# Kernel tuning notes

Measured on AMD Instinct MI355X. Metric: run time of the kernel, lower is better.

## Reference

```python
import jax, jax.numpy as jnp
import numpy as np

N_NODES = 100000
N_EDGES = 800000
IN_DIM = 128
HIDDEN = 128
CLASSES = 40


def _glorot(key, shape):
    fan_in, fan_out = shape
    lim = (6.0 / (fan_in + fan_out)) ** 0.5
    return jax.random.uniform(key, shape, jnp.float32, -lim, lim)


def setup_inputs() -> dict:
    key = jax.random.key(0)
    ks = jax.random.split(key, 8)
    x = jax.random.normal(ks[0], (N_NODES, IN_DIM), jnp.float32)
    edge_index = jax.random.randint(ks[1], (2, N_EDGES), 0, N_NODES, jnp.int64)
    # SAGEConv layer 1: lin_l (neighbor, with bias), lin_r (root, no bias)
    W1_l = _glorot(ks[2], (IN_DIM, HIDDEN))
    W1_r = _glorot(ks[3], (IN_DIM, HIDDEN))
    b1 = jnp.zeros((HIDDEN,), jnp.float32)
    # SAGEConv layer 2
    W2_l = _glorot(ks[4], (HIDDEN, CLASSES))
    W2_r = _glorot(ks[5], (HIDDEN, CLASSES))
    b2 = jnp.zeros((CLASSES,), jnp.float32)
    return {"x": x, "edge_index": edge_index, "W1_l": W1_l, "W1_r": W1_r,
            "b1": b1, "W2_l": W2_l, "W2_r": W2_r, "b2": b2}


def _sage_conv(x, src, dst, W_l, W_r, b):
    # mean aggregation of source-node features into destination nodes
    msgs = x[src]                                             # [E, d] gather
    agg = jax.ops.segment_sum(msgs, dst, num_segments=N_NODES)  # [N, d]
    cnt = jax.ops.segment_sum(jnp.ones((src.shape[0],), x.dtype), dst,
                              num_segments=N_NODES)           # [N]
    mean = agg / jnp.maximum(cnt, 1.0)[:, None]
    return mean @ W_l + x @ W_r + b


def reference(x, edge_index, W1_l, W1_r, b1, W2_l, W2_r, b2):
    src, dst = edge_index[0], edge_index[1]
    h = _sage_conv(x, src, dst, W1_l, W1_r, b1)
    h = jax.nn.relu(h)
    # F.dropout in eval mode is the identity (deterministic reference)
    out = _sage_conv(h, src, dst, W2_l, W2_r, b2)
    return out
```

## Files before the change

kernel.cpp:

```cpp
#include <hip/hip_runtime.h>
#include <hip/hip_bf16.h>

#define N_NODES 100000
#define N_EDGES 800000
#define IN_DIM  128
#define HIDDEN  128
#define CLASSES 40
#define CAP     32
#define NSH     8
#define SLICES  100
#define EPB     8000
#define BIN_B   (NSH*SLICES)
#define CAST_B  12500
#define PACK_B  24
#define CUR_STRIDE 12544

typedef __attribute__((ext_vector_type(8))) short bf16x8;
typedef __attribute__((ext_vector_type(4))) float floatx4;
typedef __attribute__((ext_vector_type(4))) int intx4;
typedef __attribute__((ext_vector_type(4))) unsigned short ushortx4;

__device__ __forceinline__ float bf2f(unsigned short u) {
    return __uint_as_float(((unsigned int)u) << 16);
}
__device__ __forceinline__ unsigned short f2bf(float f) {
    unsigned int u = __float_as_uint(f);
    unsigned int r = 0x7fffu + ((u >> 16) & 1u);
    return (unsigned short)((u + r) >> 16);
}
__device__ __forceinline__ int curIdx(int d) { return (d & 7) * CUR_STRIDE + (d >> 3); }

__global__ void k_prep(const int* __restrict__ src, const int* __restrict__ dst,
                       int* __restrict__ cur, int* __restrict__ csr,
                       const float* __restrict__ x, unsigned short* __restrict__ A1,
                       const float* __restrict__ W1l, const float* __restrict__ W1r,
                       unsigned short* __restrict__ Bp1,
                       const float* __restrict__ W2l, const float* __restrict__ W2r,
                       unsigned short* __restrict__ Bp2) {
    int blk = blockIdx.x;
    if (blk < BIN_B) {
        int g = blk & 7;
        int slice = blk >> 3;
        const intx4* s4p = reinterpret_cast<const intx4*>(src) + slice * (EPB / 4);
        const intx4* d4p = reinterpret_cast<const intx4*>(dst) + slice * (EPB / 4);
        for (int i = threadIdx.x; i < EPB / 4; i += 256) {
            intx4 d4 = __builtin_nontemporal_load(d4p + i);
            intx4 s4 = __builtin_nontemporal_load(s4p + i);
            #pragma unroll
            for (int j = 0; j < 4; ++j) {
                int d = d4[j];
                if ((d & 7) == g) {
                    int s = s4[j];
                    int slot = atomicAdd(&cur[g * CUR_STRIDE + (d >> 3)], 1);
                    if (slot < CAP) csr[d * CAP + slot] = s;
                }
            }
        }
    } else if (blk < BIN_B + CAST_B) {
        int t = (blk - BIN_B) * 256 + threadIdx.x;
        int n = t >> 5, g = t & 31;
        floatx4 v = __builtin_nontemporal_load(
            reinterpret_cast<const floatx4*>(x + (size_t)n * 128) + g);
        ushortx4 u = { f2bf(v.x), f2bf(v.y), f2bf(v.z), f2bf(v.w) };
        __builtin_nontemporal_store(u,
            reinterpret_cast<ushortx4*>(A1 + (size_t)n * 256 + 128 + g * 4));
    } else {
        int t = (blk - BIN_B - CAST_B) * 256 + threadIdx.x;
        if (t < 4096) {
            int o = t >> 7, n = t & 127;
            const float* W = (o < 16) ? W1l : W1r;
            int k0 = (o & 15) * 8;
            union { unsigned short us[8]; uint4 v; } pk;
            #pragma unroll
            for (int j = 0; j < 8; ++j) pk.us[j] = f2bf(W[(size_t)(k0 + j) * 128 + n]);
            *(uint4*)(Bp1 + (size_t)t * 8) = pk.v;
        } else {
            int t2 = t - 4096;
            int o = t2 >> 7, n = t2 & 127;
            const float* W = (n < 64) ? W2l : W2r;
            int col = n & 63;
            int k0 = o * 8;
            union { unsigned short us[8]; uint4 v; } pk;
            #pragma unroll
            for (int j = 0; j < 8; ++j)
                pk.us[j] = (col < 40) ? f2bf(W[(size_t)(k0 + j) * 40 + col]) : (unsigned short)0;
            *(uint4*)(Bp2 + (size_t)t2 * 8) = pk.v;
        }
    }
}

__global__ void k_agg1(unsigned short* __restrict__ A1, const int* __restrict__ deg,
                       const int* __restrict__ csr) {
    int n = blockIdx.x * 4 + (threadIdx.x >> 6);
    int lane = threadIdx.x & 63;
    if (n >= N_NODES) return;
    int cnt = min(deg[curIdx(n)], CAP);
    int nl = csr[n * CAP + (lane & (CAP - 1))];
    int r = lane >> 4, c = lane & 15;
    float acc[8] = {0.f, 0.f, 0.f, 0.f, 0.f, 0.f, 0.f, 0.f};
    for (int base = 0; base < cnt; base += 16) {
        #pragma unroll
        for (int u = 0; u < 4; ++u) {
            int e = base + u * 4 + r;
            int s = __shfl(nl, min(e, cnt - 1) & 31, 64);
            bf16x8 v = {};
            if (e < cnt)
                v = *(const bf16x8*)(A1 + (size_t)s * 256 + 128 + c * 8);
            #pragma unroll
            for (int j = 0; j < 8; ++j) acc[j] += bf2f((unsigned short)v[j]);
        }
    }
    #pragma unroll
    for (int j = 0; j < 8; ++j) {
        acc[j] += __shfl_xor(acc[j], 16, 64);
        acc[j] += __shfl_xor(acc[j], 32, 64);
    }
    if (lane < 16) {
        float inv = 1.0f / fmaxf((float)cnt, 1.0f);
        union { unsigned short us[8]; bf16x8 v; } pk;
        #pragma unroll
        for (int j = 0; j < 8; ++j) pk.us[j] = f2bf(acc[j] * inv);
        *(bf16x8*)(A1 + (size_t)n * 256 + c * 8) = pk.v;
    }
}

__global__ __launch_bounds__(256)
void k_gemm(unsigned short* __restrict__ A1, const unsigned short* __restrict__ Bp1,
            const float* __restrict__ b1, const unsigned short* __restrict__ Bp2) {
    __shared__ unsigned short Hs[4][16][136];
    int wv = threadIdx.x >> 6, lane = threadIdx.x & 63;
    int q = lane >> 4, nn = lane & 15;
    int m0 = blockIdx.x * 64 + wv * 16;
    int ma = m0 + nn;
    bool mv = (ma < N_NODES);
    const unsigned short* arow = A1 + (size_t)ma * 256;

    floatx4 acc[8] = {};
    for (int kt = 0; kt < 8; ++kt) {
        bf16x8 a = {};
        if (mv) a = *(const bf16x8*)(arow + kt * 32 + q * 8);
        bf16x8 b[8];
        #pragma unroll
        for (int nt = 0; nt < 8; ++nt)
            b[nt] = *(const bf16x8*)(Bp1 + ((size_t)((kt * 4 + q) * 128 + nt * 16 + nn)) * 8);
        #pragma unroll
        for (int nt = 0; nt < 8; ++nt)
            acc[nt] = __builtin_amdgcn_mfma_f32_16x16x32_bf16(a, b[nt], acc[nt], 0, 0, 0);
    }
    #pragma unroll
    for (int nt = 0; nt < 8; ++nt) {
        int col = nt * 16 + nn;
        float bias = b1[col];
        #pragma unroll
        for (int r = 0; r < 4; ++r)
            Hs[wv][q * 4 + r][col] = f2bf(fmaxf(acc[nt][r] + bias, 0.f));
    }
    floatx4 acc2[8] = {};
    for (int kt = 0; kt < 4; ++kt) {
        bf16x8 a = *(const bf16x8*)(&Hs[wv][nn][kt * 32 + q * 8]);
        bf16x8 b[8];
        #pragma unroll
        for (int nt = 0; nt < 8; ++nt)
            b[nt] = *(const bf16x8*)(Bp2 + ((size_t)((kt * 4 + q) * 128 + nt * 16 + nn)) * 8);
        #pragma unroll
        for (int nt = 0; nt < 8; ++nt)
            acc2[nt] = __builtin_amdgcn_mfma_f32_16x16x32_bf16(a, b[nt], acc2[nt], 0, 0, 0);
    }
    #pragma unroll
    for (int nt = 0; nt < 4; ++nt) {
        int col = nt * 16 + nn;
        #pragma unroll
        for (int r = 0; r < 4; ++r) {
            int ro = m0 + q * 4 + r;
            if (ro < N_NODES)
                A1[(size_t)ro * 256 + col] = f2bf(acc2[nt][r]);
        }
    }
    #pragma unroll
    for (int nt = 4; nt < 8; ++nt) {
        int col = (nt - 4) * 16 + nn;
        #pragma unroll
        for (int r = 0; r < 4; ++r) {
            int ro = m0 + q * 4 + r;
            if (ro < N_NODES) {
                float* Rp = (float*)(A1 + (size_t)ro * 256 + 128);
                Rp[col] = acc2[nt][r];
            }
        }
    }
}

__global__ void k_agg2(const unsigned short* __restrict__ A1, const int* __restrict__ deg,
                       const int* __restrict__ csr, const float* __restrict__ b2,
                       float* __restrict__ out) {
    int n = blockIdx.x * 4 + (threadIdx.x >> 6);
    int lane = threadIdx.x & 63;
    if (n >= N_NODES) return;
    int cnt = min(deg[curIdx(n)], CAP);
    int nl = csr[n * CAP + (lane & (CAP - 1))];
    int r = lane >> 3, c = lane & 7;
    float acc[8] = {0.f, 0.f, 0.f, 0.f, 0.f, 0.f, 0.f, 0.f};
    for (int base = 0; base < cnt; base += 16) {
        #pragma unroll
        for (int u = 0; u < 2; ++u) {
            int e = base + u * 8 + r;
            int s = __shfl(nl, min(e, cnt - 1) & 31, 64);
            bf16x8 v = {};
            if (e < cnt)
                v = *(const bf16x8*)(A1 + (size_t)s * 256 + c * 8);
            #pragma unroll
            for (int j = 0; j < 8; ++j) acc[j] += bf2f((unsigned short)v[j]);
        }
    }
    #pragma unroll
    for (int j = 0; j < 8; ++j) {
        acc[j] += __shfl_xor(acc[j], 8, 64);
        acc[j] += __shfl_xor(acc[j], 16, 64);
        acc[j] += __shfl_xor(acc[j], 32, 64);
    }
    if (lane < 5) {
        float inv = 1.0f / fmaxf((float)cnt, 1.0f);
        const float* Rrow = (const float*)(A1 + (size_t)n * 256 + 128);
        float o[8];
        #pragma unroll
        for (int j = 0; j < 8; ++j)
            o[j] = acc[j] * inv + Rrow[c * 8 + j] + b2[c * 8 + j];
        float* op = out + (size_t)n * CLASSES + c * 8;
        *(float4*)(op)     = make_float4(o[0], o[1], o[2], o[3]);
        *(float4*)(op + 4) = make_float4(o[4], o[5], o[6], o[7]);
    }
}

extern "C" void kernel_launch(void* const* d_in, const int* in_sizes, int n_in,
                              void* d_out, int out_size, void* d_ws, size_t ws_size,
                              hipStream_t stream) {
    const float* x   = (const float*)d_in[0];
    const int*   ei  = (const int*)d_in[1];
    const float* W1l = (const float*)d_in[2];
    const float* W1r = (const float*)d_in[3];
    const float* b1  = (const float*)d_in[4];
    const float* W2l = (const float*)d_in[5];
    const float* W2r = (const float*)d_in[6];
    const float* b2  = (const float*)d_in[7];
    float* out = (float*)d_out;

    const int* src = ei;
    const int* dst = ei + N_EDGES;

    char* ws = (char*)d_ws;
    size_t off = 0;
    auto alloc = [&](size_t bytes) { void* p = ws + off; off += (bytes + 511) & ~(size_t)511; return p; };
    int* cur = (int*)alloc((size_t)NSH * CUR_STRIDE * 4);
    int* csr = (int*)alloc((size_t)N_NODES * CAP * 4);
    unsigned short* Bp1 = (unsigned short*)alloc((size_t)32 * 128 * 8 * 2);
    unsigned short* Bp2 = (unsigned short*)alloc((size_t)16 * 128 * 8 * 2);
    unsigned short* A1  = (unsigned short*)alloc((size_t)N_NODES * 256 * 2);

    hipMemsetAsync(cur, 0, (size_t)NSH * CUR_STRIDE * 4, stream);

    k_prep<<<BIN_B + CAST_B + PACK_B, 256, 0, stream>>>(
        src, dst, cur, csr, x, A1, W1l, W1r, Bp1, W2l, W2r, Bp2);

    k_agg1<<<(N_NODES + 3) / 4, 256, 0, stream>>>(A1, cur, csr);
    k_gemm<<<(N_NODES + 63) / 64, 256, 0, stream>>>(A1, Bp1, b1, Bp2);
    k_agg2<<<(N_NODES + 3) / 4, 256, 0, stream>>>(A1, cur, csr, b2, out);
}
```

Before: 261.4 us.

## Split interleaved activation buffer into separate compact arrays and split cast kernel

Replaces the single interleaved 256-wide A1 buffer with separate contiguous buffers for the bf16 input, the layer-1 mean, the layer-2 projected features and the fp32 root term. Gathers in both aggregation kernels now read from dense rows with a smaller stride, which should improve cache-line and TLB locality. The x-to-bf16 cast moves out of the fused prep kernel into its own launch, and the aggregation loops unroll less. The cost is an extra launch and a larger workspace, and the cast no longer overlaps the edge binning inside one grid.

```diff
diff --git a/kernel.cpp b/kernel.cpp
--- a/kernel.cpp
+++ b/kernel.cpp
@@ -11,14 +11,13 @@
 #define SLICES  100
 #define EPB     8000
 #define BIN_B   (NSH*SLICES)
+#define PACK_B  24
 #define CAST_B  12500
-#define PACK_B  24
 #define CUR_STRIDE 12544
 
 typedef __attribute__((ext_vector_type(8))) short bf16x8;
 typedef __attribute__((ext_vector_type(4))) float floatx4;
 typedef __attribute__((ext_vector_type(4))) int intx4;
-typedef __attribute__((ext_vector_type(4))) unsigned short ushortx4;
 
 __device__ __forceinline__ float bf2f(unsigned short u) {
     return __uint_as_float(((unsigned int)u) << 16);
@@ -30,13 +29,12 @@
 }
 __device__ __forceinline__ int curIdx(int d) { return (d & 7) * CUR_STRIDE + (d >> 3); }
 
-__global__ void k_prep(const int* __restrict__ src, const int* __restrict__ dst,
-                       int* __restrict__ cur, int* __restrict__ csr,
-                       const float* __restrict__ x, unsigned short* __restrict__ A1,
-                       const float* __restrict__ W1l, const float* __restrict__ W1r,
-                       unsigned short* __restrict__ Bp1,
-                       const float* __restrict__ W2l, const float* __restrict__ W2r,
-                       unsigned short* __restrict__ Bp2) {
+__global__ void k_bin(const int* __restrict__ src, const int* __restrict__ dst,
+                      int* __restrict__ cur, int* __restrict__ csr,
+                      const float* __restrict__ W1l, const float* __restrict__ W1r,
+                      unsigned short* __restrict__ Bp1,
+                      const float* __restrict__ W2l, const float* __restrict__ W2r,
+                      unsigned short* __restrict__ Bp2) {
     int blk = blockIdx.x;
     if (blk < BIN_B) {
         int g = blk & 7;
@@ -56,16 +54,8 @@
                 }
             }
         }
-    } else if (blk < BIN_B + CAST_B) {
+    } else {
         int t = (blk - BIN_B) * 256 + threadIdx.x;
-        int n = t >> 5, g = t & 31;
-        floatx4 v = __builtin_nontemporal_load(
-            reinterpret_cast<const floatx4*>(x + (size_t)n * 128) + g);
-        ushortx4 u = { f2bf(v.x), f2bf(v.y), f2bf(v.z), f2bf(v.w) };
-        __builtin_nontemporal_store(u,
-            reinterpret_cast<ushortx4*>(A1 + (size_t)n * 256 + 128 + g * 4));
-    } else {
-        int t = (blk - BIN_B - CAST_B) * 256 + threadIdx.x;
         if (t < 4096) {
             int o = t >> 7, n = t & 127;
             const float* W = (o < 16) ? W1l : W1r;
@@ -89,8 +79,17 @@
     }
 }
 
-__global__ void k_agg1(unsigned short* __restrict__ A1, const int* __restrict__ deg,
-                       const int* __restrict__ csr) {
+__global__ void k_cast(const float* __restrict__ x, unsigned short* __restrict__ Xbf) {
+    int t = blockIdx.x * 256 + threadIdx.x;
+    int n = t >> 5, g = t & 31;
+    float4 v = reinterpret_cast<const float4*>(x + (size_t)n * 128)[g];
+    ushort4 u = { f2bf(v.x), f2bf(v.y), f2bf(v.z), f2bf(v.w) };
+    *(ushort4*)(Xbf + (size_t)n * 128 + g * 4) = u;
+}
+
+__global__ void k_agg1(const unsigned short* __restrict__ Xbf,
+                       unsigned short* __restrict__ Mean,
+                       const int* __restrict__ deg, const int* __restrict__ csr) {
     int n = blockIdx.x * 4 + (threadIdx.x >> 6);
     int lane = threadIdx.x & 63;
     if (n >= N_NODES) return;
@@ -98,14 +97,14 @@
     int nl = csr[n * CAP + (lane & (CAP - 1))];
     int r = lane >> 4, c = lane & 15;
     float acc[8] = {0.f, 0.f, 0.f, 0.f, 0.f, 0.f, 0.f, 0.f};
-    for (int base = 0; base < cnt; base += 16) {
-        #pragma unroll
-        for (int u = 0; u < 4; ++u) {
+    for (int base = 0; base < cnt; base += 8) {
+        #pragma unroll
+        for (int u = 0; u < 2; ++u) {
             int e = base + u * 4 + r;
             int s = __shfl(nl, min(e, cnt - 1) & 31, 64);
             bf16x8 v = {};
             if (e < cnt)
-                v = *(const bf16x8*)(A1 + (size_t)s * 256 + 128 + c * 8);
+                v = *(const bf16x8*)(Xbf + (size_t)s * 128 + c * 8);
             #pragma unroll
             for (int j = 0; j < 8; ++j) acc[j] += bf2f((unsigned short)v[j]);
         }
@@ -120,25 +119,30 @@
         union { unsigned short us[8]; bf16x8 v; } pk;
         #pragma unroll
         for (int j = 0; j < 8; ++j) pk.us[j] = f2bf(acc[j] * inv);
-        *(bf16x8*)(A1 + (size_t)n * 256 + c * 8) = pk.v;
+        *(bf16x8*)(Mean + (size_t)n * 128 + c * 8) = pk.v;
     }
 }
 
 __global__ __launch_bounds__(256)
-void k_gemm(unsigned short* __restrict__ A1, const unsigned short* __restrict__ Bp1,
-            const float* __restrict__ b1, const unsigned short* __restrict__ Bp2) {
+void k_gemm(const unsigned short* __restrict__ Mean, const unsigned short* __restrict__ Xbf,
+            unsigned short* __restrict__ Pbuf, float* __restrict__ Rbuf,
+            const unsigned short* __restrict__ Bp1, const float* __restrict__ b1,
+            const unsigned short* __restrict__ Bp2) {
     __shared__ unsigned short Hs[4][16][136];
     int wv = threadIdx.x >> 6, lane = threadIdx.x & 63;
     int q = lane >> 4, nn = lane & 15;
     int m0 = blockIdx.x * 64 + wv * 16;
     int ma = m0 + nn;
     bool mv = (ma < N_NODES);
-    const unsigned short* arow = A1 + (size_t)ma * 256;
 
     floatx4 acc[8] = {};
     for (int kt = 0; kt < 8; ++kt) {
         bf16x8 a = {};
-        if (mv) a = *(const bf16x8*)(arow + kt * 32 + q * 8);
+        if (mv) {
+            const unsigned short* arow = (kt < 4) ? (Mean + (size_t)ma * 128 + kt * 32)
+                                                  : (Xbf  + (size_t)ma * 128 + (kt - 4) * 32);
+            a = *(const bf16x8*)(arow + q * 8);
+        }
         bf16x8 b[8];
         #pragma unroll
         for (int nt = 0; nt < 8; ++nt)
@@ -173,7 +177,7 @@
         for (int r = 0; r < 4; ++r) {
             int ro = m0 + q * 4 + r;
             if (ro < N_NODES)
-                A1[(size_t)ro * 256 + col] = f2bf(acc2[nt][r]);
+                Pbuf[(size_t)ro * 64 + col] = f2bf(acc2[nt][r]);
         }
     }
     #pragma unroll
@@ -182,17 +186,15 @@
         #pragma unroll
         for (int r = 0; r < 4; ++r) {
             int ro = m0 + q * 4 + r;
-            if (ro < N_NODES) {
-                float* Rp = (float*)(A1 + (size_t)ro * 256 + 128);
-                Rp[col] = acc2[nt][r];
-            }
-        }
-    }
-}
-
-__global__ void k_agg2(const unsigned short* __restrict__ A1, const int* __restrict__ deg,
-                       const int* __restrict__ csr, const float* __restrict__ b2,
-                       float* __restrict__ out) {
+            if (ro < N_NODES)
+                Rbuf[(size_t)ro * 64 + col] = acc2[nt][r];
+        }
+    }
+}
+
+__global__ void k_agg2(const unsigned short* __restrict__ Pbuf, const float* __restrict__ Rbuf,
+                       const int* __restrict__ deg, const int* __restrict__ csr,
+                       const float* __restrict__ b2, float* __restrict__ out) {
     int n = blockIdx.x * 4 + (threadIdx.x >> 6);
     int lane = threadIdx.x & 63;
     if (n >= N_NODES) return;
@@ -200,17 +202,14 @@
     int nl = csr[n * CAP + (lane & (CAP - 1))];
     int r = lane >> 3, c = lane & 7;
     float acc[8] = {0.f, 0.f, 0.f, 0.f, 0.f, 0.f, 0.f, 0.f};
-    for (int base = 0; base < cnt; base += 16) {
-        #pragma unroll
-        for (int u = 0; u < 2; ++u) {
-            int e = base + u * 8 + r;
-            int s = __shfl(nl, min(e, cnt - 1) & 31, 64);
-            bf16x8 v = {};
-            if (e < cnt)
-                v = *(const bf16x8*)(A1 + (size_t)s * 256 + c * 8);
-            #pragma unroll
-            for (int j = 0; j < 8; ++j) acc[j] += bf2f((unsigned short)v[j]);
-        }
+    for (int base = 0; base < cnt; base += 8) {
+        int e = base + r;
+        int s = __shfl(nl, min(e, cnt - 1) & 31, 64);
+        bf16x8 v = {};
+        if (e < cnt)
+            v = *(const bf16x8*)(Pbuf + (size_t)s * 64 + c * 8);
+        #pragma unroll
+        for (int j = 0; j < 8; ++j) acc[j] += bf2f((unsigned short)v[j]);
     }
     #pragma unroll
     for (int j = 0; j < 8; ++j) {
@@ -220,7 +219,7 @@
     }
     if (lane < 5) {
         float inv = 1.0f / fmaxf((float)cnt, 1.0f);
-        const float* Rrow = (const float*)(A1 + (size_t)n * 256 + 128);
+        const float* Rrow = Rbuf + (size_t)n * 64;
         float o[8];
         #pragma unroll
         for (int j = 0; j < 8; ++j)
@@ -254,14 +253,18 @@
     int* csr = (int*)alloc((size_t)N_NODES * CAP * 4);
     unsigned short* Bp1 = (unsigned short*)alloc((size_t)32 * 128 * 8 * 2);
     unsigned short* Bp2 = (unsigned short*)alloc((size_t)16 * 128 * 8 * 2);
-    unsigned short* A1  = (unsigned short*)alloc((size_t)N_NODES * 256 * 2);
+    unsigned short* Xbf  = (unsigned short*)alloc((size_t)N_NODES * 128 * 2);
+    unsigned short* Mean = (unsigned short*)alloc((size_t)N_NODES * 128 * 2);
+    unsigned short* Pbuf = (unsigned short*)alloc((size_t)N_NODES * 64 * 2);
+    float* Rbuf = (float*)alloc((size_t)N_NODES * 64 * 4);
 
     hipMemsetAsync(cur, 0, (size_t)NSH * CUR_STRIDE * 4, stream);
 
-    k_prep<<<BIN_B + CAST_B + PACK_B, 256, 0, stream>>>(
-        src, dst, cur, csr, x, A1, W1l, W1r, Bp1, W2l, W2r, Bp2);
-
-    k_agg1<<<(N_NODES + 3) / 4, 256, 0, stream>>>(A1, cur, csr);
-    k_gemm<<<(N_NODES + 63) / 64, 256, 0, stream>>>(A1, Bp1, b1, Bp2);
-    k_agg2<<<(N_NODES + 3) / 4, 256, 0, stream>>>(A1, cur, csr, b2, out);
-}
+    k_bin<<<BIN_B + PACK_B, 256, 0, stream>>>(src, dst, cur, csr,
+                                              W1l, W1r, Bp1, W2l, W2r, Bp2);
+    k_cast<<<CAST_B, 256, 0, stream>>>(x, Xbf);
+
+    k_agg1<<<(N_NODES + 3) / 4, 256, 0, stream>>>(Xbf, Mean, cur, csr);
+    k_gemm<<<(N_NODES + 63) / 64, 256, 0, stream>>>(Mean, Xbf, Pbuf, Rbuf, Bp1, b1, Bp2);
+    k_agg2<<<(N_NODES + 3) / 4, 256, 0, stream>>>(Pbuf, Rbuf, cur, csr, b2, out);
+}
```

Measured after the change: 263.6 us. Within noise of the previous version (+0.8%).
